# Kernel optimization log

Hardware: AMD Instinct MI355X
Metric: run time of the kernel (lower is better)

## Reference

```python
import jax, jax.numpy as jnp
import numpy as np

NUM_GROUPS = 16
EPS = 1e-6


def setup_inputs() -> dict:
    key = jax.random.key(0)
    k1, k2, k3, k4 = jax.random.split(key, 4)
    B, N = 16, 131072
    pred = jax.random.normal(k1, (B, N, 3), dtype=jnp.float32)
    target = jax.random.normal(k2, (B, N, 3), dtype=jnp.float32)
    mask = jax.random.randint(k3, (B, N), 0, 2, dtype=jnp.int32)
    groups = jax.random.randint(k4, (B, N), 0, NUM_GROUPS, dtype=jnp.int32)
    return {"pred": pred, "target": target, "mask": mask, "groups": groups}


def _group_median_normalizer(z, valid, groups):
    """Per-point depth normalizer: lower-median of |z| within each (batch, group)
    over valid points, clamped to EPS; groups with no valid points get 1.0.
    z, valid, groups: (B, N). Returns (B, N)."""
    gids = jnp.arange(NUM_GROUPS, dtype=groups.dtype)
    in_g = (groups[:, None, :] == gids[None, :, None]) & valid[:, None, :]  # (B,G,N)
    inf = jnp.asarray(jnp.inf, z.dtype)
    z_g = jnp.where(in_g, z[:, None, :], inf)        # (B,G,N), invalid -> +inf
    z_sorted = jnp.sort(z_g, axis=-1)                # valid values occupy first cnt slots
    cnt = jnp.sum(in_g, axis=-1)                     # (B,G)
    idx = jnp.maximum(cnt - 1, 0) // 2               # torch lower median index
    med = jnp.take_along_axis(z_sorted, idx[..., None], axis=-1)[..., 0]  # (B,G)
    # empty groups give +inf -> nan_to_num -> 1.0, matching torch's untouched default
    med = jnp.nan_to_num(med, nan=1.0, posinf=1.0, neginf=1.0)
    med_safe = jnp.maximum(jnp.abs(med), EPS)        # clamp(|median|, min=eps)
    return jnp.take_along_axis(med_safe, groups, axis=-1)  # gather per point (B,N)


def _log_transform(x):
    return jnp.sign(x) * jnp.log1p(jnp.abs(x))


def reference(pred, target, mask, groups):
    valid = mask.astype(bool)                        # (B,N)
    # shared depth normalization: denominator from TARGET, used for both
    norm = _group_median_normalizer(target[..., 2], valid, groups)  # (B,N)
    vm = valid[..., None]                            # (B,N,1)
    inv = 1.0 / norm[..., None]
    p = jnp.nan_to_num(jnp.where(vm, pred, 0.0) * inv, nan=0.0, posinf=0.0, neginf=0.0)
    t = jnp.nan_to_num(jnp.where(vm, target, 0.0) * inv, nan=0.0, posinf=0.0, neginf=0.0)
    loss = jnp.abs(_log_transform(p) - _log_transform(t))  # (B,N,3)
    loss = jnp.where(vm, loss, 0.0)
    denom = 3.0 * jnp.sum(valid).astype(jnp.float32) + 1e-6  # expanded mask count
    return jnp.sum(loss) / denom
```

## Files before the change

kernel.cpp:

```cpp
#include <hip/hip_runtime.h>
#include <math.h>

#define NPTS_N 131072
#define NGROUP 16
#define NBG 256
#define CBLK 512
#define BPB 32
#define PPB 4096
#define SEGCAP 256
#define NSEL 6144
#define NACC 64
#define LGRID 1024
#define EPSF 1e-6f

__device__ __forceinline__ unsigned f2key(float f) {
    unsigned u = __float_as_uint(f);
    return (u & 0x80000000u) ? ~u : (u | 0x80000000u);
}
__device__ __forceinline__ float key2f(unsigned k) {
    unsigned u = (k & 0x80000000u) ? (k ^ 0x80000000u) : ~k;
    return __uint_as_float(u);
}
__device__ __forceinline__ float flog1p(float a) {
    return __log2f(1.0f + a) * 0.69314718056f;
}

__global__ __launch_bounds__(256) void compact_kernel(
        const float* __restrict__ target,
        const int* __restrict__ mask,
        const int* __restrict__ groups,
        unsigned* __restrict__ bucket,
        unsigned* __restrict__ blockCnt,
        unsigned char* __restrict__ packed) {
    __shared__ unsigned scnt[NGROUP];
    int tid = threadIdx.x, blk = blockIdx.x;
    int i0 = blk * PPB + tid * 16;
    if (tid < NGROUP) scnt[tid] = 0;
    __syncthreads();
    int4 m[4], g[4];
    #pragma unroll
    for (int k = 0; k < 4; ++k) {
        m[k] = *(const int4*)(mask + i0 + k * 4);
        g[k] = *(const int4*)(groups + i0 + k * 4);
    }
    unsigned pk[4];
    unsigned keys[16]; unsigned meta[16]; unsigned vbits = 0;
    #pragma unroll
    for (int k = 0; k < 4; ++k) {
        int mm[4] = {m[k].x, m[k].y, m[k].z, m[k].w};
        int gg[4] = {g[k].x, g[k].y, g[k].z, g[k].w};
        unsigned pb = 0;
        #pragma unroll
        for (int j = 0; j < 4; ++j) {
            int idx = k * 4 + j;
            unsigned gj = (unsigned)gg[j] & 15u;
            pb |= (gj | (mm[j] ? 0x80u : 0u)) << (8 * j);
            if (mm[j]) {
                keys[idx] = f2key(target[(size_t)(i0 + idx) * 3 + 2]);
                unsigned pos = atomicAdd(&scnt[gj], 1u);
                meta[idx] = (gj << 16) | pos;
                vbits |= 1u << idx;
            }
        }
        pk[k] = pb;
    }
    *(uint4*)(packed + i0) = make_uint4(pk[0], pk[1], pk[2], pk[3]);
    __syncthreads();
    if (tid < NGROUP) blockCnt[blk * NGROUP + tid] = scnt[tid];
    #pragma unroll
    for (int idx = 0; idx < 16; ++idx) {
        if (vbits & (1u << idx)) {
            unsigned gj = meta[idx] >> 16, pos = meta[idx] & 0xFFFFu;
            if (pos < SEGCAP)
                bucket[(size_t)(blk * NGROUP + gj) * SEGCAP + pos] = keys[idx];
        }
    }
}

__global__ __launch_bounds__(256) void select_kernel(
        const unsigned* __restrict__ bucket,
        const unsigned* __restrict__ blockCnt,
        float* __restrict__ norm,
        unsigned* __restrict__ cnt,
        float* __restrict__ accF,
        unsigned* __restrict__ done) {
    __shared__ unsigned skey[NSEL];
    __shared__ unsigned hist[2048];
    __shared__ unsigned sc[BPB];
    __shared__ unsigned segoff[BPB + 1];
    __shared__ unsigned wsum[4];
    __shared__ unsigned sres[2];
    int bg = blockIdx.x, tid = threadIdx.x;
    int b = bg >> 4, g = bg & 15;
    if (bg == 0) {
        if (tid < NACC) accF[tid] = 0.f;
        if (tid == NACC) *done = 0;
    }
    if (tid < BPB) {
        unsigned s = blockCnt[(b * BPB + tid) * NGROUP + g];
        sc[tid] = s;
        unsigned inc = s;
        #pragma unroll
        for (int o = 1; o < BPB; o <<= 1) {
            unsigned v = __shfl_up(inc, o, 64);
            if (tid >= o) inc += v;
        }
        segoff[tid + 1] = inc;
        if (tid == 0) segoff[0] = 0;
    }
    __syncthreads();
    unsigned ntrue = segoff[BPB];
    unsigned n = ntrue > NSEL ? NSEL : ntrue;
    if (tid == 0) cnt[bg] = ntrue;
    if (n == 0) { if (tid == 0) norm[bg] = 1.0f; return; }
    int wv = tid >> 6, ln = tid & 63;
    for (int c = wv; c < BPB; c += 4) {
        unsigned count = sc[c], o = segoff[c];
        if (count > SEGCAP) count = SEGCAP;
        const unsigned* src = bucket + (size_t)((b * BPB + c) * NGROUP + g) * SEGCAP;
        for (unsigned j = ln; j < count; j += 64)
            if (o + j < NSEL) skey[o + j] = src[j];
    }
    __syncthreads();

    unsigned rank = (n - 1) >> 1;
    unsigned selkey = 0;
    const int shifts[3] = {21, 10, 0};
    const int widths[3] = {11, 11, 10};
    for (int p = 0; p < 3; ++p) {
        int sft = shifts[p], w = widths[p];
        unsigned nb = 1u << w, bmask = nb - 1;
        for (unsigned j = tid; j < nb; j += 256) hist[j] = 0;
        __syncthreads();
        for (unsigned j = tid; j < n; j += 256) {
            unsigned key = skey[j];
            bool in = (p == 0) || ((key >> (sft + w)) == selkey);
            if (in) atomicAdd(&hist[(key >> sft) & bmask], 1u);
        }
        __syncthreads();
        unsigned cpl = nb >> 8;
        unsigned basebin = tid * cpl;
        unsigned s = 0;
        for (unsigned j = 0; j < cpl; ++j) s += hist[basebin + j];
        unsigned inc = s;
        #pragma unroll
        for (int o = 1; o < 64; o <<= 1) {
            unsigned v = __shfl_up(inc, o, 64);
            if ((tid & 63) >= o) inc += v;
        }
        if ((tid & 63) == 63) wsum[tid >> 6] = inc;
        __syncthreads();
        unsigned woff = 0;
        for (int w2 = 0; w2 < (tid >> 6); ++w2) woff += wsum[w2];
        unsigned excl = woff + inc - s;
        if (rank >= excl && rank < excl + s) {
            unsigned run = excl, binSel = basebin;
            for (unsigned j = 0; j < cpl; ++j) {
                unsigned h = hist[basebin + j];
                if (run + h > rank) { binSel = basebin + j; break; }
                run += h;
            }
            sres[0] = binSel; sres[1] = rank - run;
        }
        __syncthreads();
        selkey = (selkey << w) | sres[0];
        rank = sres[1];
        __syncthreads();
    }
    if (tid == 0) norm[bg] = fmaxf(fabsf(key2f(selkey)), EPSF);
}

__global__ __launch_bounds__(256) void loss_kernel(
        const float* __restrict__ pred,
        const float* __restrict__ target,
        const unsigned char* __restrict__ packed,
        const float* __restrict__ norm,
        const unsigned* __restrict__ cnt,
        float* __restrict__ accF,
        unsigned* __restrict__ done,
        float* __restrict__ out) {
    __shared__ float sinv[NGROUP];
    __shared__ float swsum[4];
    __shared__ bool isLast;
    __shared__ float red[256];
    __shared__ float accSum;
    int tid = threadIdx.x;
    int blk = blockIdx.x;
    int b = blk >> 6;
    if (tid < NGROUP) sinv[tid] = 1.0f / norm[(b << 4) + tid];
    __syncthreads();
    int p0 = b * NPTS_N + (blk & 63) * 2048 + tid * 8;
    uint2 pkw = *(const uint2*)(packed + p0);
    const float4* pr4 = (const float4*)(pred + (size_t)p0 * 3);
    const float4* tg4 = (const float4*)(target + (size_t)p0 * 3);
    float pv[24], tv[24];
    #pragma unroll
    for (int k = 0; k < 6; ++k) { *(float4*)(pv + 4 * k) = pr4[k]; *(float4*)(tv + 4 * k) = tg4[k]; }
    float acc = 0.f;
    #pragma unroll
    for (int q = 0; q < 8; ++q) {
        unsigned byte = ((q < 4 ? pkw.x : pkw.y) >> (8 * (q & 3))) & 0xFFu;
        if (byte & 0x80u) {
            float inv = sinv[byte & 15u];
            #pragma unroll
            for (int c = 0; c < 3; ++c) {
                float pp = pv[q * 3 + c] * inv;
                float tt = tv[q * 3 + c] * inv;
                float lp = copysignf(flog1p(fabsf(pp)), pp);
                float lt = copysignf(flog1p(fabsf(tt)), tt);
                acc += fabsf(lp - lt);
            }
        }
    }
    #pragma unroll
    for (int off = 32; off; off >>= 1) acc += __shfl_down(acc, off, 64);
    if ((tid & 63) == 0) swsum[tid >> 6] = acc;
    __syncthreads();
    if (tid == 0) {
        float v = swsum[0] + swsum[1] + swsum[2] + swsum[3];
        atomicAdd(&accF[blk & (NACC - 1)], v);
        __asm__ volatile("s_waitcnt vmcnt(0)" ::: "memory");
        unsigned old = __hip_atomic_fetch_add(done, 1u, __ATOMIC_RELAXED,
                                              __HIP_MEMORY_SCOPE_AGENT);
        isLast = (old == (unsigned)(LGRID - 1));
    }
    __syncthreads();
    if (isLast) {
        float s = 0.f;
        if (tid < NACC)
            s = __hip_atomic_load(&accF[tid], __ATOMIC_RELAXED, __HIP_MEMORY_SCOPE_AGENT);
        #pragma unroll
        for (int off = 32; off; off >>= 1) s += __shfl_down(s, off, 64);
        if (tid == 0) accSum = s;
        red[tid] = (float)cnt[tid];
        __syncthreads();
        for (int st = 128; st; st >>= 1) {
            if (tid < st) red[tid] += red[tid + st];
            __syncthreads();
        }
        if (tid == 0) out[0] = accSum / (3.0f * red[0] + 1e-6f);
    }
}

extern "C" void kernel_launch(void* const* d_in, const int* in_sizes, int n_in,
                              void* d_out, int out_size, void* d_ws, size_t ws_size,
                              hipStream_t stream) {
    const float* pred   = (const float*)d_in[0];
    const float* target = (const float*)d_in[1];
    const int*   mask   = (const int*)d_in[2];
    const int*   groups = (const int*)d_in[3];
    float* out = (float*)d_out;

    char* ws = (char*)d_ws;
    const size_t MB = 1024 * 1024;
    unsigned*      bucket   = (unsigned*)ws;
    unsigned char* packed   = (unsigned char*)(ws + 8 * MB);
    unsigned*      blockCnt = (unsigned*)(ws + 10 * MB);
    unsigned*      cnt      = (unsigned*)(ws + 10 * MB + 32768);
    float*         normv    = (float*)(ws + 10 * MB + 32768 + 1024);
    float*         accF     = (float*)(ws + 10 * MB + 32768 + 2048);
    unsigned*      done     = (unsigned*)(ws + 10 * MB + 32768 + 3072);

    compact_kernel<<<dim3(CBLK), dim3(256), 0, stream>>>(target, mask, groups,
                                                         bucket, blockCnt, packed);
    select_kernel<<<dim3(NBG), dim3(256), 0, stream>>>(bucket, blockCnt, normv, cnt, accF, done);
    loss_kernel<<<dim3(LGRID), dim3(256), 0, stream>>>(pred, target, packed, normv,
                                                       cnt, accF, done, out);
}
```

Before: 133.3 us.

## Stream radix-select first pass from global buckets and keep only survivors in LDS

The select kernel no longer copies every group's keys into a 24KB shared array. The first histogram pass reads keys straight from the global buckets, then a second global pass compacts only keys matching the selected top bin into a small 8KB shared buffer. If more than 2048 keys survive, it falls back to rescanning global memory. This cuts shared memory per block, which may raise occupancy, but reads the buckets twice and adds an atomic compaction step. The loss kernel's packed-byte extraction now uses a single 64-bit load and shift.

```diff
diff --git a/kernel.cpp b/kernel.cpp
--- a/kernel.cpp
+++ b/kernel.cpp
@@ -8,7 +8,7 @@
 #define BPB 32
 #define PPB 4096
 #define SEGCAP 256
-#define NSEL 6144
+#define SK2CAP 2048
 #define NACC 64
 #define LGRID 1024
 #define EPSF 1e-6f
@@ -84,47 +84,39 @@
         unsigned* __restrict__ cnt,
         float* __restrict__ accF,
         unsigned* __restrict__ done) {
-    __shared__ unsigned skey[NSEL];
     __shared__ unsigned hist[2048];
+    __shared__ unsigned skey2[SK2CAP];
     __shared__ unsigned sc[BPB];
-    __shared__ unsigned segoff[BPB + 1];
     __shared__ unsigned wsum[4];
     __shared__ unsigned sres[2];
+    __shared__ unsigned sn[2];
+    __shared__ unsigned m2;
     int bg = blockIdx.x, tid = threadIdx.x;
     int b = bg >> 4, g = bg & 15;
+    int wv = tid >> 6, ln = tid & 63;
     if (bg == 0) {
         if (tid < NACC) accF[tid] = 0.f;
         if (tid == NACC) *done = 0;
     }
-    if (tid < BPB) {
-        unsigned s = blockCnt[(b * BPB + tid) * NGROUP + g];
-        sc[tid] = s;
-        unsigned inc = s;
-        #pragma unroll
-        for (int o = 1; o < BPB; o <<= 1) {
-            unsigned v = __shfl_up(inc, o, 64);
-            if (tid >= o) inc += v;
-        }
-        segoff[tid + 1] = inc;
-        if (tid == 0) segoff[0] = 0;
-    }
-    __syncthreads();
-    unsigned ntrue = segoff[BPB];
-    unsigned n = ntrue > NSEL ? NSEL : ntrue;
-    if (tid == 0) cnt[bg] = ntrue;
+    if (tid < BPB) sc[tid] = blockCnt[(b * BPB + tid) * NGROUP + g];
+    __syncthreads();
+    if (tid == 0) {
+        unsigned ntrue = 0, ncap = 0;
+        for (int c = 0; c < BPB; ++c) {
+            unsigned s = sc[c];
+            ntrue += s;
+            ncap += (s > SEGCAP ? SEGCAP : s);
+        }
+        sn[0] = ntrue; sn[1] = ncap;
+        cnt[bg] = ntrue;
+    }
+    __syncthreads();
+    unsigned n = sn[1];
     if (n == 0) { if (tid == 0) norm[bg] = 1.0f; return; }
-    int wv = tid >> 6, ln = tid & 63;
-    for (int c = wv; c < BPB; c += 4) {
-        unsigned count = sc[c], o = segoff[c];
-        if (count > SEGCAP) count = SEGCAP;
-        const unsigned* src = bucket + (size_t)((b * BPB + c) * NGROUP + g) * SEGCAP;
-        for (unsigned j = ln; j < count; j += 64)
-            if (o + j < NSEL) skey[o + j] = src[j];
-    }
-    __syncthreads();
 
     unsigned rank = (n - 1) >> 1;
     unsigned selkey = 0;
+    unsigned m2cnt = 0; bool ovf = false;
     const int shifts[3] = {21, 10, 0};
     const int widths[3] = {11, 11, 10};
     for (int p = 0; p < 3; ++p) {
@@ -132,10 +124,29 @@
         unsigned nb = 1u << w, bmask = nb - 1;
         for (unsigned j = tid; j < nb; j += 256) hist[j] = 0;
         __syncthreads();
-        for (unsigned j = tid; j < n; j += 256) {
-            unsigned key = skey[j];
-            bool in = (p == 0) || ((key >> (sft + w)) == selkey);
-            if (in) atomicAdd(&hist[(key >> sft) & bmask], 1u);
+        if (p == 0) {
+            for (int c = wv * 8; c < wv * 8 + 8; ++c) {
+                unsigned count = sc[c]; if (count > SEGCAP) count = SEGCAP;
+                const unsigned* src = bucket + (size_t)((b * BPB + c) * NGROUP + g) * SEGCAP;
+                for (unsigned j = ln; j < count; j += 64)
+                    atomicAdd(&hist[src[j] >> 21], 1u);
+            }
+        } else if (!ovf) {
+            for (unsigned j = tid; j < m2cnt; j += 256) {
+                unsigned key = skey2[j];
+                bool in = (p == 1) || ((key >> 10) == selkey);
+                if (in) atomicAdd(&hist[(key >> sft) & bmask], 1u);
+            }
+        } else {
+            for (int c = wv * 8; c < wv * 8 + 8; ++c) {
+                unsigned count = sc[c]; if (count > SEGCAP) count = SEGCAP;
+                const unsigned* src = bucket + (size_t)((b * BPB + c) * NGROUP + g) * SEGCAP;
+                for (unsigned j = ln; j < count; j += 64) {
+                    unsigned key = src[j];
+                    if ((key >> (sft + w)) == selkey)
+                        atomicAdd(&hist[(key >> sft) & bmask], 1u);
+                }
+            }
         }
         __syncthreads();
         unsigned cpl = nb >> 8;
@@ -166,6 +177,26 @@
         selkey = (selkey << w) | sres[0];
         rank = sres[1];
         __syncthreads();
+        if (p == 0) {
+            if (tid == 0) m2 = 0;
+            __syncthreads();
+            for (int c = wv * 8; c < wv * 8 + 8; ++c) {
+                unsigned count = sc[c]; if (count > SEGCAP) count = SEGCAP;
+                const unsigned* src = bucket + (size_t)((b * BPB + c) * NGROUP + g) * SEGCAP;
+                for (unsigned j = ln; j < count; j += 64) {
+                    unsigned key = src[j];
+                    if ((key >> 21) == selkey) {
+                        unsigned pos = atomicAdd(&m2, 1u);
+                        if (pos < SK2CAP) skey2[pos] = key;
+                    }
+                }
+            }
+            __syncthreads();
+            m2cnt = m2;
+            ovf = (m2cnt > SK2CAP);
+            if (ovf) m2cnt = 0;
+            __syncthreads();
+        }
     }
     if (tid == 0) norm[bg] = fmaxf(fabsf(key2f(selkey)), EPSF);
 }
@@ -190,7 +221,7 @@
     if (tid < NGROUP) sinv[tid] = 1.0f / norm[(b << 4) + tid];
     __syncthreads();
     int p0 = b * NPTS_N + (blk & 63) * 2048 + tid * 8;
-    uint2 pkw = *(const uint2*)(packed + p0);
+    unsigned long long pk64 = *(const unsigned long long*)(packed + p0);
     const float4* pr4 = (const float4*)(pred + (size_t)p0 * 3);
     const float4* tg4 = (const float4*)(target + (size_t)p0 * 3);
     float pv[24], tv[24];
@@ -199,7 +230,7 @@
     float acc = 0.f;
     #pragma unroll
     for (int q = 0; q < 8; ++q) {
-        unsigned byte = ((q < 4 ? pkw.x : pkw.y) >> (8 * (q & 3))) & 0xFFu;
+        unsigned byte = (unsigned)(pk64 >> (8 * q)) & 0xFFu;
         if (byte & 0x80u) {
             float inv = sinv[byte & 15u];
             #pragma unroll
@@ -263,7 +294,8 @@
 
     compact_kernel<<<dim3(CBLK), dim3(256), 0, stream>>>(target, mask, groups,
                                                          bucket, blockCnt, packed);
-    select_kernel<<<dim3(NBG), dim3(256), 0, stream>>>(bucket, blockCnt, normv, cnt, accF, done);
+    select_kernel<<<dim3(NBG), dim3(256), 0, stream>>>(bucket, blockCnt, normv,
+                                                       cnt, accF, done);
     loss_kernel<<<dim3(LGRID), dim3(256), 0, stream>>>(pred, target, packed, normv,
                                                        cnt, accF, done, out);
 }
```

After: 133.5 us. Within noise of the previous version (+0.1%).
